# Performance work log

Measured on AMD Instinct MI355X. Metric: run time of the kernel, lower is better.

The kernel has to match this reference:

```python
import jax, jax.numpy as jnp
import numpy as np

FI_BIT, FI_GROUP = 8, 64
FW_BIT, FW_GROUP = 8, 64


def quantize_bfp(x, bit, group):
    """Block-floating-point quantize: groups of `group` elems along the last dim
    share the exponent of the group max; mantissas are rounded to `bit` bits."""
    shp = x.shape
    xg = x.reshape(shp[:-1] + (shp[-1] // group, group))
    maxabs = jnp.max(jnp.abs(xg), axis=-1, keepdims=True)
    e = jnp.floor(jnp.log2(jnp.maximum(maxabs, jnp.asarray(1e-38, x.dtype))))
    step = jnp.exp2(e - (bit - 1))  # quantization step for shared exponent e
    qmax = 2 ** (bit - 1) - 1
    q = jnp.clip(jnp.round(xg / step), -(qmax + 1), qmax) * step
    q = jnp.where(maxabs == 0, jnp.zeros_like(q), q)
    return q.reshape(shp)


def setup_inputs() -> dict:
    key = jax.random.key(0)
    k1, k2, k3 = jax.random.split(key, 3)
    N, IN, OUT = 4096, 4096, 4096
    x = jax.random.normal(k1, (N, IN), dtype=jnp.float32)
    # weight/bias initialized uniform(-0.1, 0.1) as in the torch module
    weight = jax.random.uniform(k2, (OUT, IN), dtype=jnp.float32, minval=-0.1, maxval=0.1)
    bias = jax.random.uniform(k3, (OUT,), dtype=jnp.float32, minval=-0.1, maxval=0.1)
    return {"x": x, "weight": weight, "bias": bias}


def reference(x, weight, bias):
    xq = quantize_bfp(x, FI_BIT, FI_GROUP)          # [N, IN]
    wq = quantize_bfp(weight, FW_BIT, FW_GROUP)     # [OUT, IN]
    out = jnp.einsum('ni,oi->no', xq, wq)
    # Faithful to the original forward: F.linear adds bias once, then the
    # explicit `output += bias` adds it a second time.
    out = out + 2.0 * bias[None, :]
    return out
```

## Files before the change

kernel.cpp:

```cpp
#include <hip/hip_runtime.h>
#include <stdint.h>

typedef __bf16 bf16_t;
typedef __attribute__((ext_vector_type(8))) __bf16 bf16x8;
typedef __attribute__((ext_vector_type(4))) float f32x4;

#define NDIM 4096

__global__ __launch_bounds__(256) void quant_bfp(const float* __restrict__ in0,
                                                 bf16_t* __restrict__ out0,
                                                 const float* __restrict__ in1,
                                                 bf16_t* __restrict__ out1) {
    const float* in = blockIdx.y ? in1 : in0;
    bf16_t* out     = blockIdx.y ? out1 : out0;
    const int t = blockIdx.x * 256 + threadIdx.x;
    float4 v = ((const float4*)in)[t];
    float m = fmaxf(fmaxf(fabsf(v.x), fabsf(v.y)), fmaxf(fabsf(v.z), fabsf(v.w)));
    m = fmaxf(m, __shfl_xor(m, 1));
    m = fmaxf(m, __shfl_xor(m, 2));
    m = fmaxf(m, __shfl_xor(m, 4));
    m = fmaxf(m, __shfl_xor(m, 8));
    const int e = (int)((__float_as_uint(m) >> 23) & 0xFF) - 127;
    float step = __uint_as_float((uint32_t)(e + 120) << 23);
    float inv  = __uint_as_float((uint32_t)(134 - e) << 23);
    if (m == 0.0f) { step = 0.0f; inv = 0.0f; }
    float q0 = fminf(fmaxf(rintf(v.x * inv), -128.0f), 127.0f) * step;
    float q1 = fminf(fmaxf(rintf(v.y * inv), -128.0f), 127.0f) * step;
    float q2 = fminf(fmaxf(rintf(v.z * inv), -128.0f), 127.0f) * step;
    float q3 = fminf(fmaxf(rintf(v.w * inv), -128.0f), 127.0f) * step;
    union { bf16_t b[4]; uint2 u; } o;
    o.b[0] = (bf16_t)q0; o.b[1] = (bf16_t)q1;
    o.b[2] = (bf16_t)q2; o.b[3] = (bf16_t)q3;
    ((uint2*)out)[t] = o.u;
}

__device__ __forceinline__ void g2l16(const bf16_t* g, void* l) {
    __builtin_amdgcn_global_load_lds(
        (__attribute__((address_space(1))) void*)g,
        (__attribute__((address_space(3))) void*)l, 16, 0, 0);
}

__global__ __launch_bounds__(256) void gemm_bfp(const bf16_t* __restrict__ A,
                                                const bf16_t* __restrict__ B,
                                                const float* __restrict__ bias,
                                                float* __restrict__ C) {
    __shared__ bf16_t sA[128 * 64];
    __shared__ bf16_t sB[128 * 64];

    const int tid  = threadIdx.x;
    const int wave = tid >> 6;
    const int lane = tid & 63;
    const int bm = blockIdx.y, bn = blockIdx.x;
    const int m_wave = (wave >> 1) * 64;
    const int n_wave = (wave & 1) * 64;

    const int srow = tid >> 3;
    const int swz  = (((tid & 7) ^ (srow & 7)) * 8);
    const bf16_t* gA = A + (size_t)(bm * 128) * NDIM + swz;
    const bf16_t* gB = B + (size_t)(bn * 128) * NDIM + swz;

    f32x4 acc[4][4];
#pragma unroll
    for (int i = 0; i < 4; ++i)
#pragma unroll
        for (int j = 0; j < 4; ++j)
            acc[i][j] = (f32x4){0.0f, 0.0f, 0.0f, 0.0f};

    const int quad = lane >> 4;
    const int l16  = lane & 15;
    const int rsw  = l16 & 7;

    for (int kt = 0; kt < NDIM; kt += 64) {
#pragma unroll
        for (int i = 0; i < 4; ++i) {
            const bf16_t* g = gA + (size_t)(i * 32 + srow) * NDIM + kt;
            g2l16(g, (char*)sA + i * 4096 + tid * 16);
        }
#pragma unroll
        for (int i = 0; i < 4; ++i) {
            const bf16_t* g = gB + (size_t)(i * 32 + srow) * NDIM + kt;
            g2l16(g, (char*)sB + i * 4096 + tid * 16);
        }
        __syncthreads();

#pragma unroll
        for (int ks = 0; ks < 64; ks += 32) {
            const int ce = (((ks >> 3) + quad) ^ rsw) * 8;
            bf16x8 af[4], bfr[4];
#pragma unroll
            for (int i = 0; i < 4; ++i)
                af[i] = *(const bf16x8*)&sA[(m_wave + i * 16 + l16) * 64 + ce];
#pragma unroll
            for (int j = 0; j < 4; ++j)
                bfr[j] = *(const bf16x8*)&sB[(n_wave + j * 16 + l16) * 64 + ce];
#pragma unroll
            for (int i = 0; i < 4; ++i)
#pragma unroll
                for (int j = 0; j < 4; ++j)
                    acc[i][j] = __builtin_amdgcn_mfma_f32_16x16x32_bf16(
                        af[i], bfr[j], acc[i][j], 0, 0, 0);
        }
        __syncthreads();
    }

    const int row0 = bm * 128 + m_wave + quad * 4;
    const int col0 = bn * 128 + n_wave + l16;
#pragma unroll
    for (int j = 0; j < 4; ++j) {
        const int c = col0 + j * 16;
        const float bv = 2.0f * bias[c];
#pragma unroll
        for (int i = 0; i < 4; ++i) {
            const int r = row0 + i * 16;
#pragma unroll
            for (int reg = 0; reg < 4; ++reg)
                C[(size_t)(r + reg) * NDIM + c] = acc[i][j][reg] + bv;
        }
    }
}

extern "C" void kernel_launch(void* const* d_in, const int* in_sizes, int n_in,
                              void* d_out, int out_size, void* d_ws, size_t ws_size,
                              hipStream_t stream) {
    const float* x    = (const float*)d_in[0];
    const float* w    = (const float*)d_in[1];
    const float* bias = (const float*)d_in[2];
    float* out = (float*)d_out;

    bf16_t* xq = (bf16_t*)d_ws;
    bf16_t* wq = xq + (size_t)NDIM * NDIM;

    const int qblocks = (NDIM * NDIM / 4) / 256;
    dim3 qgrid(qblocks, 2);
    quant_bfp<<<qgrid, 256, 0, stream>>>(x, xq, w, wq);

    dim3 grid(NDIM / 128, NDIM / 128);
    gemm_bfp<<<grid, 256, 0, stream>>>(xq, wq, bias, out);
}
```

Measured before the change: 305.7 us.

## Widen quantize to 8 elems per thread, swizzle GEMM block order, precompute pointers

The quantize kernel now processes 8 floats per thread with two float4 loads, one 16-byte store and one fewer shuffle step, which halves the thread count and widens memory transactions. The GEMM remaps block indices so groups of consecutive blocks share A/B tiles for better L2 reuse. It also replaces per-iteration address recomputation with incrementing row pointers and precomputed swizzle offsets. These cut address arithmetic and cache misses, at the cost of slightly more registers for the pointer arrays.

Measured after the change: 300.5 us. About the same (-1.7%).

```diff
diff --git a/kernel.cpp b/kernel.cpp
--- a/kernel.cpp
+++ b/kernel.cpp
@@ -14,24 +14,23 @@
     const float* in = blockIdx.y ? in1 : in0;
     bf16_t* out     = blockIdx.y ? out1 : out0;
     const int t = blockIdx.x * 256 + threadIdx.x;
-    float4 v = ((const float4*)in)[t];
-    float m = fmaxf(fmaxf(fabsf(v.x), fabsf(v.y)), fmaxf(fabsf(v.z), fabsf(v.w)));
+    float4 a = ((const float4*)in)[2 * t];
+    float4 b = ((const float4*)in)[2 * t + 1];
+    float m = fmaxf(fmaxf(fmaxf(fabsf(a.x), fabsf(a.y)), fmaxf(fabsf(a.z), fabsf(a.w))),
+                    fmaxf(fmaxf(fabsf(b.x), fabsf(b.y)), fmaxf(fabsf(b.z), fabsf(b.w))));
     m = fmaxf(m, __shfl_xor(m, 1));
     m = fmaxf(m, __shfl_xor(m, 2));
     m = fmaxf(m, __shfl_xor(m, 4));
-    m = fmaxf(m, __shfl_xor(m, 8));
     const int e = (int)((__float_as_uint(m) >> 23) & 0xFF) - 127;
     float step = __uint_as_float((uint32_t)(e + 120) << 23);
     float inv  = __uint_as_float((uint32_t)(134 - e) << 23);
     if (m == 0.0f) { step = 0.0f; inv = 0.0f; }
-    float q0 = fminf(fmaxf(rintf(v.x * inv), -128.0f), 127.0f) * step;
-    float q1 = fminf(fmaxf(rintf(v.y * inv), -128.0f), 127.0f) * step;
-    float q2 = fminf(fmaxf(rintf(v.z * inv), -128.0f), 127.0f) * step;
-    float q3 = fminf(fmaxf(rintf(v.w * inv), -128.0f), 127.0f) * step;
-    union { bf16_t b[4]; uint2 u; } o;
-    o.b[0] = (bf16_t)q0; o.b[1] = (bf16_t)q1;
-    o.b[2] = (bf16_t)q2; o.b[3] = (bf16_t)q3;
-    ((uint2*)out)[t] = o.u;
+    float q[8] = {a.x, a.y, a.z, a.w, b.x, b.y, b.z, b.w};
+    union { bf16_t h[8]; uint4 u; } o;
+#pragma unroll
+    for (int i = 0; i < 8; ++i)
+        o.h[i] = (bf16_t)(fminf(fmaxf(rintf(q[i] * inv), -128.0f), 127.0f) * step);
+    ((uint4*)out)[t] = o.u;
 }
 
 __device__ __forceinline__ void g2l16(const bf16_t* g, void* l) {
@@ -50,14 +49,24 @@
     const int tid  = threadIdx.x;
     const int wave = tid >> 6;
     const int lane = tid & 63;
-    const int bm = blockIdx.y, bn = blockIdx.x;
+
+    const int p  = blockIdx.y * 32 + blockIdx.x;
+    const int bn = ((p & 7) << 2) | ((p >> 3) & 3);
+    const int bm = p >> 5;
+
     const int m_wave = (wave >> 1) * 64;
     const int n_wave = (wave & 1) * 64;
 
     const int srow = tid >> 3;
     const int swz  = (((tid & 7) ^ (srow & 7)) * 8);
-    const bf16_t* gA = A + (size_t)(bm * 128) * NDIM + swz;
-    const bf16_t* gB = B + (size_t)(bn * 128) * NDIM + swz;
+
+    const bf16_t* pA[4];
+    const bf16_t* pB[4];
+#pragma unroll
+    for (int i = 0; i < 4; ++i) {
+        pA[i] = A + (size_t)(bm * 128 + i * 32 + srow) * NDIM + swz;
+        pB[i] = B + (size_t)(bn * 128 + i * 32 + srow) * NDIM + swz;
+    }
 
     f32x4 acc[4][4];
 #pragma unroll
@@ -69,23 +78,25 @@
     const int quad = lane >> 4;
     const int l16  = lane & 15;
     const int rsw  = l16 & 7;
+    const int ce0  = (quad ^ rsw) * 8;
+    const int ce1  = ((4 + quad) ^ rsw) * 8;
 
     for (int kt = 0; kt < NDIM; kt += 64) {
 #pragma unroll
         for (int i = 0; i < 4; ++i) {
-            const bf16_t* g = gA + (size_t)(i * 32 + srow) * NDIM + kt;
-            g2l16(g, (char*)sA + i * 4096 + tid * 16);
+            g2l16(pA[i], (char*)sA + i * 4096 + tid * 16);
+            pA[i] += 64;
         }
 #pragma unroll
         for (int i = 0; i < 4; ++i) {
-            const bf16_t* g = gB + (size_t)(i * 32 + srow) * NDIM + kt;
-            g2l16(g, (char*)sB + i * 4096 + tid * 16);
+            g2l16(pB[i], (char*)sB + i * 4096 + tid * 16);
+            pB[i] += 64;
         }
         __syncthreads();
 
 #pragma unroll
         for (int ks = 0; ks < 64; ks += 32) {
-            const int ce = (((ks >> 3) + quad) ^ rsw) * 8;
+            const int ce = ks ? ce1 : ce0;
             bf16x8 af[4], bfr[4];
 #pragma unroll
             for (int i = 0; i < 4; ++i)
@@ -130,7 +141,7 @@
     bf16_t* xq = (bf16_t*)d_ws;
     bf16_t* wq = xq + (size_t)NDIM * NDIM;
 
-    const int qblocks = (NDIM * NDIM / 4) / 256;
+    const int qblocks = (NDIM * NDIM / 8) / 256;
     dim3 qgrid(qblocks, 2);
     quant_bfp<<<qgrid, 256, 0, stream>>>(x, xq, w, wq);
 
```
